# Kernel tuning notes

Measured on AMD Instinct MI355X. Metric: run time of the kernel, lower is better.

Reference implementation:

```python
import jax, jax.numpy as jnp
import numpy as np

B, H, W = 8, 64, 64
DIM, NH, WS = 384, 6, 14
HD = DIM // NH
MLP = int(DIM * 4.0)
EPS = 1e-5
SCALE = HD ** -0.5


def setup_inputs() -> dict:
    key = jax.random.key(0)
    ks = jax.random.split(key, 8)
    init = lambda k, shape: (jax.random.normal(k, shape, dtype=jnp.float32) * 0.02)
    return {
        "x": jax.random.normal(ks[0], (B, H, W, DIM), dtype=jnp.float32),
        "ln1_w": jnp.ones((DIM,), jnp.float32),
        "ln1_b": jnp.zeros((DIM,), jnp.float32),
        "qkv_w": init(ks[1], (DIM, 3 * DIM)),
        "qkv_b": jnp.zeros((3 * DIM,), jnp.float32),
        "proj_w": init(ks[2], (DIM, DIM)),
        "proj_b": jnp.zeros((DIM,), jnp.float32),
        "rel_pos_h": init(ks[3], (2 * WS - 1, HD)),
        "rel_pos_w": init(ks[4], (2 * WS - 1, HD)),
        "ln2_w": jnp.ones((DIM,), jnp.float32),
        "ln2_b": jnp.zeros((DIM,), jnp.float32),
        "fc1_w": init(ks[5], (DIM, MLP)),
        "fc1_b": jnp.zeros((MLP,), jnp.float32),
        "fc2_w": init(ks[6], (MLP, DIM)),
        "fc2_b": jnp.zeros((DIM,), jnp.float32),
    }


def _layernorm(x, w, b):
    m = x.mean(-1, keepdims=True)
    v = ((x - m) ** 2).mean(-1, keepdims=True)
    return (x - m) * jax.lax.rsqrt(v + EPS) * w + b


def _get_rel_pos(rel_pos, ws):
    # q_size == k_size == ws and rel_pos has 2*ws-1 rows, so torch's
    # F.interpolate to max_rel_dist=2*ws-1 is an identity; direct indexing.
    coords = jnp.arange(ws)[:, None] - jnp.arange(ws)[None, :] + (ws - 1)
    return rel_pos[coords]  # (ws, ws, head_dim)


def _attention(xw, qkv_w, qkv_b, proj_w, proj_b, rel_pos_h, rel_pos_w):
    Bw = xw.shape[0]
    N = WS * WS
    qkv = xw.reshape(Bw, N, DIM) @ qkv_w + qkv_b  # (Bw, N, 3*DIM)
    qkv = qkv.reshape(Bw, N, 3, NH, HD).transpose(2, 0, 3, 1, 4).reshape(3, Bw * NH, N, HD)
    q, k, v = qkv[0], qkv[1], qkv[2]
    attn = jnp.einsum("bqd,bkd->bqk", q * SCALE, k)  # (Bw*NH, N, N)
    Rh = _get_rel_pos(rel_pos_h, WS)
    Rw = _get_rel_pos(rel_pos_w, WS)
    rq = q.reshape(Bw * NH, WS, WS, HD)
    rel_h = jnp.einsum("bhwc,hkc->bhwk", rq, Rh)
    rel_w = jnp.einsum("bhwc,wkc->bhwk", rq, Rw)
    attn = (attn.reshape(Bw * NH, WS, WS, WS, WS)
            + rel_h[:, :, :, :, None]
            + rel_w[:, :, :, None, :]).reshape(Bw * NH, N, N)
    attn = jax.nn.softmax(attn, axis=-1)
    out = jnp.einsum("bqk,bkd->bqd", attn, v)
    out = out.reshape(Bw, NH, WS, WS, HD).transpose(0, 2, 3, 1, 4).reshape(Bw, WS, WS, DIM)
    return out @ proj_w + proj_b


def reference(x, ln1_w, ln1_b, qkv_w, qkv_b, proj_w, proj_b, rel_pos_h, rel_pos_w,
              ln2_w, ln2_b, fc1_w, fc1_b, fc2_w, fc2_b):
    shortcut = x
    h = _layernorm(x, ln1_w, ln1_b)
    pad_h = (WS - H % WS) % WS
    pad_w = (WS - W % WS) % WS
    Hp, Wp = H + pad_h, W + pad_w
    hp = jnp.pad(h, ((0, 0), (0, pad_h), (0, pad_w), (0, 0)))
    # window partition: (B, Hp, Wp, C) -> (B*nWin, WS, WS, C)
    wins = hp.reshape(B, Hp // WS, WS, Wp // WS, WS, DIM)
    wins = wins.transpose(0, 1, 3, 2, 4, 5).reshape(-1, WS, WS, DIM)
    wins = _attention(wins, qkv_w, qkv_b, proj_w, proj_b, rel_pos_h, rel_pos_w)
    # window unpartition
    y = wins.reshape(B, Hp // WS, Wp // WS, WS, WS, DIM)
    y = y.transpose(0, 1, 3, 2, 4, 5).reshape(B, Hp, Wp, DIM)[:, :H, :W, :]
    x = shortcut + y
    h2 = _layernorm(x, ln2_w, ln2_b)
    mlp = jax.nn.gelu(h2 @ fc1_w + fc1_b, approximate=False) @ fc2_w + fc2_b
    return x + mlp
```

## Files before the change

### kernel.cpp

```cpp
#include <hip/hip_runtime.h>
#include <math.h>

#define DIMC 384
#define NHD  6
#define HD   64
#define WSZ  14
#define NTOK 196
#define NWIN 200
#define NWH  1200
#define MWIN 39200
#define MX   32768
#define MLPD 1536

typedef short short8 __attribute__((ext_vector_type(8)));
typedef float f32x4 __attribute__((ext_vector_type(4)));
typedef float f32x16 __attribute__((ext_vector_type(16)));

__device__ __forceinline__ unsigned short f2bf(float f) {
  unsigned int u = __float_as_uint(f);
  u = (u + 0x7fffu + ((u >> 16) & 1u)) >> 16;
  return (unsigned short)u;
}
__device__ __forceinline__ float bf2f(unsigned int u) {
  return __uint_as_float(u << 16);
}
__device__ __forceinline__ unsigned int pkbf(float a, float b) {
  unsigned int r; asm("v_cvt_pk_bf16_f32 %0, %1, %2" : "=v"(r) : "v"(a), "v"(b)); return r;
}
__device__ __forceinline__ float gelu_t(float x) {
  float z = 1.5957691216057308f * (x + 0.044715f * x * x * x);
  float e = __expf(z);
  float th = 1.f - 2.f * __builtin_amdgcn_rcpf(e + 1.f);
  return 0.5f * x * (1.f + th);
}

typedef const __attribute__((address_space(1))) unsigned int* gptr_t;
typedef __attribute__((address_space(3))) unsigned int* lptr_t;
__device__ __forceinline__ void gload16(const unsigned short* g, unsigned short* l) {
  __builtin_amdgcn_global_load_lds((gptr_t)(const void*)g, (lptr_t)(void*)l, 16, 0, 0);
}

#define LN1BLKS 9800
#define SEG0 442368
#define SEG1 589824
#define SEG2 1179648
#define SEG3 1769472
#define SEG4 1773568
#define SEG5 2003968
__global__ __launch_bounds__(256) void pre_kernel(
    const float* __restrict__ x, const float* __restrict__ ln1w, const float* __restrict__ ln1b,
    const float* __restrict__ qkvw, const float* __restrict__ projw,
    const float* __restrict__ fc1w, const float* __restrict__ fc2w,
    const float* __restrict__ relh, const float* __restrict__ relw,
    unsigned short* __restrict__ xw,
    unsigned short* __restrict__ qkvwT, unsigned short* __restrict__ projwT,
    unsigned short* __restrict__ fc1wT, unsigned short* __restrict__ fc2wT,
    unsigned short* __restrict__ relcat, unsigned short* __restrict__ vT) {
  const int blk = blockIdx.x;
  if (blk < LN1BLKS) {
    int t = blk * 4 + (threadIdx.x >> 6);
    int lane = threadIdx.x & 63;
    int win = t / NTOK, p = t - win * NTOK;
    int bb = win / 25, rem = win - bb * 25;
    int wi = rem / 5, wj = rem - wi * 5;
    int i = p / WSZ, j = p - i * WSZ;
    int r = wi * WSZ + i, c = wj * WSZ + j;
    unsigned short* o = xw + (size_t)t * DIMC;
    if (r >= 64 || c >= 64) {
      #pragma unroll
      for (int q = 0; q < 6; q++) o[lane + q * 64] = 0;
      return;
    }
    const float* xr = x + (((size_t)bb * 64 + r) * 64 + c) * DIMC;
    float v[6]; float s = 0.f, s2 = 0.f;
    #pragma unroll
    for (int q = 0; q < 6; q++) { float f = xr[lane + q * 64]; v[q] = f; s += f; s2 += f * f; }
    #pragma unroll
    for (int off = 32; off; off >>= 1) { s += __shfl_xor(s, off); s2 += __shfl_xor(s2, off); }
    float mean = s * (1.f / DIMC);
    float var  = s2 * (1.f / DIMC) - mean * mean;
    float rstd = rsqrtf(var + 1e-5f);
    #pragma unroll
    for (int q = 0; q < 6; q++) {
      int d = lane + q * 64;
      o[d] = f2bf((v[q] - mean) * rstd * ln1w[d] + ln1b[d]);
    }
    return;
  }
  int id = (blk - LN1BLKS) * 256 + threadIdx.x;
  if (id < SEG0) {
    int n = id / 384, k = id - n * 384;
    qkvwT[id] = f2bf(qkvw[(size_t)k * 1152 + n]);
  } else if (id < SEG1) {
    id -= SEG0;
    int n = id / 384, k = id - n * 384;
    projwT[id] = f2bf(projw[(size_t)k * 384 + n]);
  } else if (id < SEG2) {
    id -= SEG1;
    int n = id / 384, k = id - n * 384;
    fc1wT[id] = f2bf(fc1w[(size_t)k * 1536 + n]);
  } else if (id < SEG3) {
    id -= SEG2;
    int n = id / 1536, k = id - n * 1536;
    fc2wT[id] = f2bf(fc2w[(size_t)k * 384 + n]);
  } else if (id < SEG4) {
    id -= SEG3;
    int rc = id >> 6, d = id & 63;
    float v = 0.f;
    if (rc < 27) v = relh[rc * 64 + d] * 8.f;
    else if (rc < 54) v = relw[(rc - 27) * 64 + d] * 8.f;
    relcat[id] = f2bf(v);
  } else if (id < SEG5) {
    id -= SEG4;
    int row = id / 3, part = id - row * 3;
    *(int2*)(vT + (size_t)row * 208 + 196 + part * 4) = make_int2(0, 0);
  }
}

__global__ __launch_bounds__(256) void ln2_kernel(const unsigned short* __restrict__ x2b,
    const float* __restrict__ w, const float* __restrict__ b, unsigned short* __restrict__ h2) {
  int t = blockIdx.x * 4 + (threadIdx.x >> 6);
  int lane = threadIdx.x & 63;
  const unsigned short* xr = x2b + (size_t)t * DIMC;
  unsigned short* o = h2 + (size_t)t * DIMC;
  float v[6]; float s = 0.f, s2 = 0.f;
  #pragma unroll
  for (int q = 0; q < 6; q++) { float f = bf2f(xr[lane + q * 64]); v[q] = f; s += f; s2 += f * f; }
  #pragma unroll
  for (int off = 32; off; off >>= 1) { s += __shfl_xor(s, off); s2 += __shfl_xor(s2, off); }
  float mean = s * (1.f / DIMC);
  float var  = s2 * (1.f / DIMC) - mean * mean;
  float rstd = rsqrtf(var + 1e-5f);
  #pragma unroll
  for (int q = 0; q < 6; q++) {
    int d = lane + q * 64;
    o[d] = f2bf((v[q] - mean) * rstd * w[d] + b[d]);
  }
}

template <int EPI>
__global__ __launch_bounds__(256) void gemm_kernel(
    const unsigned short* __restrict__ A, const unsigned short* __restrict__ WT,
    int Mrows, int Kd,
    const float* __restrict__ bias,
    const float* __restrict__ addinf, const unsigned short* __restrict__ addinb,
    float* __restrict__ outf, unsigned short* __restrict__ outb,
    unsigned short* __restrict__ outb2) {
  __shared__ unsigned short As[3][128 * 32];
  __shared__ unsigned short Bs[3][128 * 32];
  const int nwg = gridDim.x * gridDim.y;
  const int flat = blockIdx.y * gridDim.x + blockIdx.x;
  const int xcd = flat & 7, q_ = nwg >> 3, r_ = nwg & 7;
  const int wg = (xcd < r_ ? xcd * (q_ + 1) : r_ * (q_ + 1) + (xcd - r_) * q_) + (flat >> 3);
  const int bx = wg / gridDim.y, by = wg - bx * gridDim.y;
  const int row0 = bx * 128, col0 = by * 128;
  const int tid = threadIdx.x;
  const int l = tid & 63, wid = tid >> 6;
  const int fr = l & 15, fk = (l >> 4) * 8;
  const int wr = (wid >> 1) * 64, wc = (wid & 1) * 64;
  const int sr = l >> 2, sc = (l & 3) * 8;
  const int scs = sc ^ (((sr >> 1) & 3) << 3);
  const int rsw = ((fr >> 1) & 3) << 3;
  f32x4 acc[4][4] = {};
  const unsigned short* ap = A + (size_t)row0 * Kd;
  const unsigned short* bp = WT + (size_t)col0 * Kd;
  const int nt = Kd >> 5;

  auto stage = [&](int t, int b) {
    const int k0 = t * 32;
    #pragma unroll
    for (int j = 0; j < 2; j++) {
      int chunk = j * 4 + wid;
      gload16(ap + (size_t)(chunk * 16 + sr) * Kd + k0 + scs, &As[b][chunk * 512]);
      gload16(bp + (size_t)(chunk * 16 + sr) * Kd + k0 + scs, &Bs[b][chunk * 512]);
    }
  };
  stage(0, 0);
  stage(1, 1);
  int c = 0;
  for (int t = 0; t < nt; ++t) {
    if (t < nt - 1) asm volatile("s_waitcnt vmcnt(4)" ::: "memory");
    else            asm volatile("s_waitcnt vmcnt(0)" ::: "memory");
    __builtin_amdgcn_s_barrier();
    __builtin_amdgcn_sched_barrier(0);
    if (t + 2 < nt) stage(t + 2, (c + 2 >= 3) ? c - 1 : c + 2);
    short8 a[4], b[4];
    #pragma unroll
    for (int fi = 0; fi < 4; fi++) {
      a[fi] = *(const short8*)&As[c][(wr + fi * 16 + fr) * 32 + (fk ^ rsw)];
      b[fi] = *(const short8*)&Bs[c][(wc + fi * 16 + fr) * 32 + (fk ^ rsw)];
    }
    __builtin_amdgcn_s_setprio(1);
    #pragma unroll
    for (int fi = 0; fi < 4; fi++)
      #pragma unroll
      for (int fj = 0; fj < 4; fj++)
        acc[fi][fj] = __builtin_amdgcn_mfma_f32_16x16x32_bf16(b[fj], a[fi], acc[fi][fj], 0, 0, 0);
    __builtin_amdgcn_s_setprio(0);
    c = (c + 1 >= 3) ? 0 : c + 1;
  }
  #pragma unroll
  for (int fi = 0; fi < 4; fi++) {
    const int gr = row0 + wr + fi * 16 + fr;
    if (gr >= Mrows) continue;
    int wv_ = 0, p = 0, valid = 1; size_t pixbase = 0;
    if (EPI == 0 || EPI == 1) { wv_ = gr / NTOK; p = gr - wv_ * NTOK; }
    if (EPI == 1) {
      int bb = wv_ / 25, rem2 = wv_ - bb * 25;
      int wi = rem2 / 5, wj = rem2 - wi * 5;
      int i = p / WSZ, j = p - i * WSZ;
      int rr = wi * WSZ + i, cc = wj * WSZ + j;
      valid = (rr < 64) && (cc < 64);
      pixbase = (((size_t)bb * 64 + rr) * 64 + cc) * DIMC;
    }
    #pragma unroll
    for (int fj = 0; fj < 4; fj++) {
      const int gcb = col0 + wc + fj * 16 + (l >> 4) * 4;
      f32x4 v = acc[fi][fj];
      float4 bv = *(const float4*)&bias[gcb];
      float t0 = v[0] + bv.x, t1 = v[1] + bv.y, t2 = v[2] + bv.z, t3 = v[3] + bv.w;
      if (EPI == 0) {
        int s = gcb / 384, rem = gcb - s * 384;
        int hh = rem >> 6, d0 = gcb & 63;
        int whh = wv_ * NHD + hh;
        if (s == 0) { t0 *= 0.125f; t1 *= 0.125f; t2 *= 0.125f; t3 *= 0.125f; }
        if (s < 2) {
          *(int2*)&outb[((size_t)s * NWH + whh) * (NTOK * 64) + p * 64 + d0] =
              make_int2((int)pkbf(t0, t1), (int)pkbf(t2, t3));
        } else {
          unsigned short* vb = outb2 + ((size_t)whh * 64 + d0) * 208 + p;
          vb[0] = f2bf(t0); vb[208] = f2bf(t1); vb[416] = f2bf(t2); vb[624] = f2bf(t3);
        }
      } else if (EPI == 1) {
        if (valid) {
          size_t idx = pixbase + gcb;
          float4 ad = *(const float4*)&addinf[idx];
          *(int2*)&outb[idx] = make_int2((int)pkbf(t0 + ad.x, t1 + ad.y),
                                         (int)pkbf(t2 + ad.z, t3 + ad.w));
        }
      } else if (EPI == 2) {
        *(int2*)&outb[(size_t)gr * MLPD + gcb] =
            make_int2((int)pkbf(gelu_t(t0), gelu_t(t1)), (int)pkbf(gelu_t(t2), gelu_t(t3)));
      } else {
        size_t idx = (size_t)gr * DIMC + gcb;
        int2 adp = *(const int2*)&addinb[idx];
        unsigned int u0 = (unsigned int)adp.x, u1 = (unsigned int)adp.y;
        float4 o = make_float4(t0 + bf2f(u0 & 0xffffu), t1 + bf2f(u0 >> 16),
                               t2 + bf2f(u1 & 0xffffu), t3 + bf2f(u1 >> 16));
        *(float4*)&outf[idx] = o;
      }
    }
  }
}

template <bool TAIL>
__device__ __forceinline__ void attn_chunk(
    int kk, int l31, int hi,
    const unsigned short* __restrict__ kg,
    const unsigned short* __restrict__ VT,
    const short8* qf, const short8* qrel,
    f32x16& olo, f32x16& ohi_, float& m_reg, float& s_run) {
  int key = kk * 32 + l31;
  int keyc = (TAIL && key > 195) ? 195 : key;
  f32x16 S = {};
  __builtin_amdgcn_s_setprio(1);
  #pragma unroll
  for (int m = 0; m < 4; m++) {
    short8 kf = *(const short8*)(kg + (size_t)keyc * 64 + m * 16 + hi * 8);
    S = __builtin_amdgcn_mfma_f32_32x32x16_bf16(kf, qf[m], S, 0, 0, 0);
  }
  {
    int ki = keyc / 14, kj = keyc - ki * 14;
    #pragma unroll
    for (int m2 = 0; m2 < 2; m2++) {
      short8 kh;
      #pragma unroll
      for (int j = 0; j < 8; j++) {
        int cc = m2 * 16 + hi * 8 + j;
        kh[j] = (short)((cc == ki || cc == 14 + kj) ? 0x3F80 : 0);
      }
      S = __builtin_amdgcn_mfma_f32_32x32x16_bf16(kh, qrel[m2], S, 0, 0, 0);
    }
  }
  __builtin_amdgcn_s_setprio(0);
  float pmax = -3e38f;
  #pragma unroll
  for (int r = 0; r < 16; r++) {
    if (TAIL) {
      int krow = kk * 32 + (r & 3) + 8 * (r >> 2) + 4 * hi;
      if (krow >= 196) S[r] = -3e38f;
    }
    pmax = fmaxf(pmax, S[r]);
  }
  pmax = fmaxf(pmax, __shfl_xor(pmax, 32));
  if (__any(pmax > m_reg + 8.f)) {
    float m_new = fmaxf(m_reg, pmax);
    float fac = __expf(m_reg - m_new);
    m_reg = m_new;
    s_run *= fac;
    #pragma unroll
    for (int r = 0; r < 16; r++) {
      int qr = (r & 3) + 8 * (r >> 2) + 4 * hi;
      float fr_ = __shfl(fac, qr);
      olo[r] *= fr_; ohi_[r] *= fr_;
    }
  }
  float psum = 0.f;
  #pragma unroll
  for (int r = 0; r < 16; r++) { S[r] = __expf(S[r] - m_reg); psum += S[r]; }
  s_run += psum;
  unsigned int pk[8];
  #pragma unroll
  for (int t = 0; t < 8; t++) pk[t] = pkbf(S[2 * t], S[2 * t + 1]);
  #pragma unroll
  for (int m2 = 0; m2 < 2; m2++) {
    int b_ = m2 * 4;
    unsigned int x0 = (unsigned int)__shfl_xor((int)pk[b_ + 0], 32);
    unsigned int x1 = (unsigned int)__shfl_xor((int)pk[b_ + 1], 32);
    unsigned int x2 = (unsigned int)__shfl_xor((int)pk[b_ + 2], 32);
    unsigned int x3 = (unsigned int)__shfl_xor((int)pk[b_ + 3], 32);
    unsigned int au[4];
    au[0] = hi ? x2 : pk[b_ + 0];
    au[1] = hi ? x3 : pk[b_ + 1];
    au[2] = hi ? pk[b_ + 2] : x0;
    au[3] = hi ? pk[b_ + 3] : x1;
    short8 pa; __builtin_memcpy(&pa, au, 16);
    int kb = kk * 32 + m2 * 16 + hi * 8;
    if (TAIL && kb > 208) kb = 208;
    short8 vblo = *(const short8*)&VT[l31 * 216 + kb];
    short8 vbhi = *(const short8*)&VT[(32 + l31) * 216 + kb];
    __builtin_amdgcn_s_setprio(1);
    olo  = __builtin_amdgcn_mfma_f32_32x32x16_bf16(pa, vblo, olo, 0, 0, 0);
    ohi_ = __builtin_amdgcn_mfma_f32_32x32x16_bf16(pa, vbhi, ohi_, 0, 0, 0);
    __builtin_amdgcn_s_setprio(0);
  }
}

__global__ __launch_bounds__(256) void attn32_kernel(
    const unsigned short* __restrict__ qk_g,
    const unsigned short* __restrict__ vT_g,
    const unsigned short* __restrict__ relcat,
    unsigned short* __restrict__ attnout) {
  __shared__ __align__(16) unsigned short VT[64 * 216];
  __shared__ __align__(16) unsigned short RELB[4][2048];
  const int wh = blockIdx.x, y = blockIdx.y;
  const int w = wh / NHD, h = wh - w * NHD;
  const int tid = threadIdx.x;
  const unsigned short* vrow = vT_g + (size_t)wh * 64 * 208;
  for (int e = tid; e < 64 * 27; e += 256) {
    int d = e / 27, c = e - d * 27;
    int4 val = {0, 0, 0, 0};
    if (c < 26) val = *(const int4*)(vrow + d * 208 + c * 8);
    *(int4*)&VT[d * 216 + c * 8] = val;
  }
  __syncthreads();
  const int l = tid & 63, wv = tid >> 6;
  const int l31 = l & 31, hi = l >> 5;
  unsigned short* RB = &RELB[wv][0];
  const unsigned short* qg = qk_g + (size_t)wh * (NTOK * 64);
  const unsigned short* kg = qk_g + (size_t)(NWH + wh) * (NTOK * 64);

  const int tbeg = y ? 4 : 0, tend = y ? 7 : 4;
  for (int tile = tbeg + wv; tile < tend; tile += 4) {
    const int q0 = tile * 32;
    int qrow = q0 + l31; if (qrow > 195) qrow = 195;
    short8 qf[4];
    #pragma unroll
    for (int m = 0; m < 4; m++)
      qf[m] = *(const short8*)(qg + (size_t)qrow * 64 + m * 16 + hi * 8);
    #pragma unroll
    for (int rt = 0; rt < 2; rt++) {
      f32x16 cr = {};
      __builtin_amdgcn_s_setprio(1);
      #pragma unroll
      for (int m = 0; m < 4; m++) {
        short8 af = *(const short8*)(relcat + (rt * 32 + l31) * 64 + m * 16 + hi * 8);
        cr = __builtin_amdgcn_mfma_f32_32x32x16_bf16(af, qf[m], cr, 0, 0, 0);
      }
      __builtin_amdgcn_s_setprio(0);
      #pragma unroll
      for (int t = 0; t < 8; t++) {
        int rr = rt * 32 + ((2 * t) & 3) + 8 * (t >> 1) + 4 * hi;
        *(unsigned int*)&RB[l31 * 64 + rr] = pkbf(cr[2 * t], cr[2 * t + 1]);
      }
    }
    __builtin_amdgcn_wave_barrier();
    int qi = qrow / 14, qj = qrow - qi * 14;
    short8 qrel[2];
    #pragma unroll
    for (int m2 = 0; m2 < 2; m2++)
      #pragma unroll
      for (int j = 0; j < 8; j++) {
        int cc = m2 * 16 + hi * 8 + j;
        unsigned short vv = 0;
        if (cc < 14) vv = RB[l31 * 64 + (qi - cc + 13)];
        else if (cc < 28) vv = RB[l31 * 64 + 27 + (qj - (cc - 14) + 13)];
        qrel[m2][j] = (short)vv;
      }
    __builtin_amdgcn_wave_barrier();
    f32x16 olo = {}, ohi_ = {};
    float m_reg = -3e38f, s_run = 0.f;
    for (int kk = 0; kk < 6; kk++)
      attn_chunk<false>(kk, l31, hi, kg, VT, qf, qrel, olo, ohi_, m_reg, s_run);
    attn_chunk<true>(6, l31, hi, kg, VT, qf, qrel, olo, ohi_, m_reg, s_run);
    s_run += __shfl_xor(s_run, 32);
    float inv = 1.f / s_run;
    #pragma unroll
    for (int r = 0; r < 16; r++) {
      int qr = (r & 3) + 8 * (r >> 2) + 4 * hi;
      float ir = __shfl(inv, qr);
      int tok = q0 + qr;
      if (tok < 196) {
        size_t base = ((size_t)w * NTOK + tok) * DIMC + h * 64;
        attnout[base + l31] = f2bf(olo[r] * ir);
        attnout[base + 32 + l31] = f2bf(ohi_[r] * ir);
      }
    }
  }
}

extern "C" void kernel_launch(void* const* d_in, const int* in_sizes, int n_in,
                              void* d_out, int out_size, void* d_ws, size_t ws_size,
                              hipStream_t stream) {
  const float* x     = (const float*)d_in[0];
  const float* ln1w  = (const float*)d_in[1];
  const float* ln1b  = (const float*)d_in[2];
  const float* qkvw  = (const float*)d_in[3];
  const float* qkvb  = (const float*)d_in[4];
  const float* projw = (const float*)d_in[5];
  const float* projb = (const float*)d_in[6];
  const float* relh  = (const float*)d_in[7];
  const float* relw  = (const float*)d_in[8];
  const float* ln2w  = (const float*)d_in[9];
  const float* ln2b  = (const float*)d_in[10];
  const float* fc1w  = (const float*)d_in[11];
  const float* fc1b  = (const float*)d_in[12];
  const float* fc2w  = (const float*)d_in[13];
  const float* fc2b  = (const float*)d_in[14];

  const size_t R0 = 0;
  const size_t R1 = R0 + 50331648;
  const size_t R2 = R1 + 100663296;
  const size_t R3 = R2 + 30408704;
  const size_t NEED = R3 + 3547136;
  if (ws_size < NEED) return;
  char* ws = (char*)d_ws;
  unsigned short* xw     = (unsigned short*)(ws + R0);
  unsigned short* x2b    = (unsigned short*)(ws + R0);
  unsigned short* qk_g   = (unsigned short*)(ws + R1);
  unsigned short* vT_g   = qk_g + (size_t)2 * NWH * NTOK * 64;
  unsigned short* hidden = (unsigned short*)(ws + R1);
  unsigned short* attno  = (unsigned short*)(ws + R2);
  unsigned short* h2     = (unsigned short*)(ws + R2);
  unsigned short* qkvwT  = (unsigned short*)(ws + R3);
  unsigned short* projwT = qkvwT + 442368;
  unsigned short* fc1wT  = projwT + 147456;
  unsigned short* fc2wT  = fc1wT + 589824;
  unsigned short* relcat = fc2wT + 589824;

  pre_kernel<<<LN1BLKS + 7828, 256, 0, stream>>>(x, ln1w, ln1b, qkvw, projw, fc1w, fc2w,
                                                 relh, relw, xw, qkvwT, projwT, fc1wT,
                                                 fc2wT, relcat, vT_g);
  gemm_kernel<0><<<dim3(307, 9), 256, 0, stream>>>(xw, qkvwT, MWIN, 384, qkvb,
                                                   nullptr, nullptr, nullptr, qk_g, vT_g);
  attn32_kernel<<<dim3(NWH, 2), 256, 0, stream>>>(qk_g, vT_g, relcat, attno);
  gemm_kernel<1><<<dim3(307, 3), 256, 0, stream>>>(attno, projwT, MWIN, 384, projb,
                                                   x, nullptr, nullptr, x2b, nullptr);
  ln2_kernel<<<8192, 256, 0, stream>>>(x2b, ln2w, ln2b, h2);
  gemm_kernel<2><<<dim3(256, 12), 256, 0, stream>>>(h2, fc1wT, MX, 384, fc1b,
                                                    nullptr, nullptr, nullptr, hidden, nullptr);
  gemm_kernel<3><<<dim3(256, 3), 256, 0, stream>>>(hidden, fc2wT, MX, 1536, fc2b,
                                                   nullptr, x2b, (float*)d_out, nullptr, nullptr);
}
```

Measured before the change: 340.5 us.

## Template GEMM row tile, use 256-row tiles for QKV and FC1, double-buffer

Makes the GEMM row-tile height a template parameter and launches the QKV and FC1 GEMMs with 256-row tiles, which halves their grid size and raises reuse of each weight tile loaded. It also replaces the three-stage LDS ring with explicit vmcnt waits by a simpler two-buffer scheme with __syncthreads. Larger tiles mean more accumulator registers and fewer workgroups, which may lower occupancy. The shallower pipeline may expose more global-load latency.

New measurement: 423.5 us. 1.24x slower.

```diff
diff --git a/kernel.cpp b/kernel.cpp
--- a/kernel.cpp
+++ b/kernel.cpp
@@ -138,7 +138,7 @@
   }
 }
 
-template <int EPI>
+template <int EPI, int TM>
 __global__ __launch_bounds__(256) void gemm_kernel(
     const unsigned short* __restrict__ A, const unsigned short* __restrict__ WT,
     int Mrows, int Kd,
@@ -146,22 +146,23 @@
     const float* __restrict__ addinf, const unsigned short* __restrict__ addinb,
     float* __restrict__ outf, unsigned short* __restrict__ outb,
     unsigned short* __restrict__ outb2) {
-  __shared__ unsigned short As[3][128 * 32];
-  __shared__ unsigned short Bs[3][128 * 32];
+  constexpr int NFI = TM / 32;
+  __shared__ unsigned short As[2][TM * 32];
+  __shared__ unsigned short Bs[2][128 * 32];
   const int nwg = gridDim.x * gridDim.y;
   const int flat = blockIdx.y * gridDim.x + blockIdx.x;
   const int xcd = flat & 7, q_ = nwg >> 3, r_ = nwg & 7;
   const int wg = (xcd < r_ ? xcd * (q_ + 1) : r_ * (q_ + 1) + (xcd - r_) * q_) + (flat >> 3);
   const int bx = wg / gridDim.y, by = wg - bx * gridDim.y;
-  const int row0 = bx * 128, col0 = by * 128;
+  const int row0 = bx * TM, col0 = by * 128;
   const int tid = threadIdx.x;
   const int l = tid & 63, wid = tid >> 6;
   const int fr = l & 15, fk = (l >> 4) * 8;
-  const int wr = (wid >> 1) * 64, wc = (wid & 1) * 64;
+  const int wr = (wid >> 1) * (TM / 2), wc = (wid & 1) * 64;
   const int sr = l >> 2, sc = (l & 3) * 8;
   const int scs = sc ^ (((sr >> 1) & 3) << 3);
   const int rsw = ((fr >> 1) & 3) << 3;
-  f32x4 acc[4][4] = {};
+  f32x4 acc[NFI][4] = {};
   const unsigned short* ap = A + (size_t)row0 * Kd;
   const unsigned short* bp = WT + (size_t)col0 * Kd;
   const int nt = Kd >> 5;
@@ -169,38 +170,40 @@
   auto stage = [&](int t, int b) {
     const int k0 = t * 32;
     #pragma unroll
+    for (int j = 0; j < TM / 64; j++) {
+      int chunk = j * 4 + wid;
+      gload16(ap + (size_t)(chunk * 16 + sr) * Kd + k0 + scs, &As[b][chunk * 512]);
+    }
+    #pragma unroll
     for (int j = 0; j < 2; j++) {
       int chunk = j * 4 + wid;
-      gload16(ap + (size_t)(chunk * 16 + sr) * Kd + k0 + scs, &As[b][chunk * 512]);
       gload16(bp + (size_t)(chunk * 16 + sr) * Kd + k0 + scs, &Bs[b][chunk * 512]);
     }
   };
   stage(0, 0);
-  stage(1, 1);
-  int c = 0;
+  __syncthreads();
+  int cur = 0;
   for (int t = 0; t < nt; ++t) {
-    if (t < nt - 1) asm volatile("s_waitcnt vmcnt(4)" ::: "memory");
-    else            asm volatile("s_waitcnt vmcnt(0)" ::: "memory");
-    __builtin_amdgcn_s_barrier();
-    __builtin_amdgcn_sched_barrier(0);
-    if (t + 2 < nt) stage(t + 2, (c + 2 >= 3) ? c - 1 : c + 2);
-    short8 a[4], b[4];
-    #pragma unroll
-    for (int fi = 0; fi < 4; fi++) {
-      a[fi] = *(const short8*)&As[c][(wr + fi * 16 + fr) * 32 + (fk ^ rsw)];
-      b[fi] = *(const short8*)&Bs[c][(wc + fi * 16 + fr) * 32 + (fk ^ rsw)];
-    }
+    if (t + 1 < nt) stage(t + 1, cur ^ 1);
+    short8 a[NFI], b[4];
+    #pragma unroll
+    for (int fi = 0; fi < NFI; fi++)
+      a[fi] = *(const short8*)&As[cur][(wr + fi * 16 + fr) * 32 + (fk ^ rsw)];
+    #pragma unroll
+    for (int fj = 0; fj < 4; fj++)
+      b[fj] = *(const short8*)&Bs[cur][(wc + fj * 16 + fr) * 32 + (fk ^ rsw)];
     __builtin_amdgcn_s_setprio(1);
     #pragma unroll
-    for (int fi = 0; fi < 4; fi++)
+    for (int fi = 0; fi < NFI; fi++)
       #pragma unroll
       for (int fj = 0; fj < 4; fj++)
         acc[fi][fj] = __builtin_amdgcn_mfma_f32_16x16x32_bf16(b[fj], a[fi], acc[fi][fj], 0, 0, 0);
     __builtin_amdgcn_s_setprio(0);
-    c = (c + 1 >= 3) ? 0 : c + 1;
-  }
-  #pragma unroll
-  for (int fi = 0; fi < 4; fi++) {
+    __syncthreads();
+    cur ^= 1;
+  }
+  #pragma unroll
+  for (int fi = 0; fi < NFI; fi++) {
     const int gr = row0 + wr + fi * 16 + fr;
     if (gr >= Mrows) continue;
     int wv_ = 0, p = 0, valid = 1; size_t pixbase = 0;
@@ -461,14 +464,14 @@
   pre_kernel<<<LN1BLKS + 7828, 256, 0, stream>>>(x, ln1w, ln1b, qkvw, projw, fc1w, fc2w,
                                                  relh, relw, xw, qkvwT, projwT, fc1wT,
                                                  fc2wT, relcat, vT_g);
-  gemm_kernel<0><<<dim3(307, 9), 256, 0, stream>>>(xw, qkvwT, MWIN, 384, qkvb,
-                                                   nullptr, nullptr, nullptr, qk_g, vT_g);
+  gemm_kernel<0, 256><<<dim3(154, 9), 256, 0, stream>>>(xw, qkvwT, MWIN, 384, qkvb,
+                                                        nullptr, nullptr, nullptr, qk_g, vT_g);
   attn32_kernel<<<dim3(NWH, 2), 256, 0, stream>>>(qk_g, vT_g, relcat, attno);
-  gemm_kernel<1><<<dim3(307, 3), 256, 0, stream>>>(attno, projwT, MWIN, 384, projb,
-                                                   x, nullptr, nullptr, x2b, nullptr);
+  gemm_kernel<1, 128><<<dim3(307, 3), 256, 0, stream>>>(attno, projwT, MWIN, 384, projb,
+                                                        x, nullptr, nullptr, x2b, nullptr);
   ln2_kernel<<<8192, 256, 0, stream>>>(x2b, ln2w, ln2b, h2);
-  gemm_kernel<2><<<dim3(256, 12), 256, 0, stream>>>(h2, fc1wT, MX, 384, fc1b,
-                                                    nullptr, nullptr, nullptr, hidden, nullptr);
-  gemm_kernel<3><<<dim3(256, 3), 256, 0, stream>>>(hidden, fc2wT, MX, 1536, fc2b,
-                                                   nullptr, x2b, (float*)d_out, nullptr, nullptr);
-}
+  gemm_kernel<2, 256><<<dim3(128, 12), 256, 0, stream>>>(h2, fc1wT, MX, 384, fc1b,
+                                                         nullptr, nullptr, nullptr, hidden, nullptr);
+  gemm_kernel<3, 128><<<dim3(256, 3), 256, 0, stream>>>(hidden, fc2wT, MX, 1536, fc2b,
+                                                        nullptr, x2b, (float*)d_out, nullptr, nullptr);
+}
```
